# Performance work log

Measured on AMD Instinct MI355X. Metric: run time of the kernel, lower is better.

The kernel has to match this reference:

```python
import jax, jax.numpy as jnp
import numpy as np

EPS = 1e-5
GROUPS = 32


def group_norm(x, gamma, beta):
    # x: [B, C, H, W], normalize per group over (C/G, H, W)
    B, C, H, W = x.shape
    xg = x.reshape(B, GROUPS, C // GROUPS, H, W)
    mean = xg.mean(axis=(2, 3, 4), keepdims=True)
    var = xg.var(axis=(2, 3, 4), keepdims=True)
    xg = (xg - mean) * jax.lax.rsqrt(var + EPS)
    x = xg.reshape(B, C, H, W)
    return x * gamma[None, :, None, None] + beta[None, :, None, None]


def setup_inputs() -> dict:
    key = jax.random.key(0)
    ks = jax.random.split(key, 6)
    B, C, H, W = 8, 512, 64, 64
    x = jax.random.normal(ks[0], (B, C, H, W), dtype=jnp.float32)
    gamma = jnp.ones((C,), dtype=jnp.float32)
    beta = jnp.zeros((C,), dtype=jnp.float32)
    # conv1x1 weights stored as [out, in] (kernel size 1 squeezed)
    w_qkv = jax.random.normal(ks[1], (3 * C, C), dtype=jnp.float32) / np.sqrt(C)
    b_qkv = jnp.zeros((3 * C,), dtype=jnp.float32)
    w_out = jax.random.normal(ks[2], (C, C), dtype=jnp.float32) / np.sqrt(C)
    b_out = jnp.zeros((C,), dtype=jnp.float32)
    return {"x": x, "gamma": gamma, "beta": beta,
            "w_qkv": w_qkv, "b_qkv": b_qkv, "w_out": w_out, "b_out": b_out}


def reference(x, gamma, beta, w_qkv, b_qkv, w_out, b_out):
    B, C, H, W = x.shape
    N = H * W
    h = group_norm(x, gamma, beta).reshape(B, C, N)
    # conv1d kernel-size-1: channel mixing
    qkv = jnp.einsum('oc,bcn->bon', w_qkv, h) + b_qkv[None, :, None]
    q, k, v = jnp.split(qkv, 3, axis=1)  # each [B, C, N]
    scale = 1.0 / jnp.sqrt(jnp.float32(C))
    attn = jnp.einsum('bci,bcj->bij', q, k) * scale  # [B, N, N]
    attn = jax.nn.softmax(attn, axis=-1)
    out = jnp.einsum('bcj,bij->bci', v, attn)  # [B, C, N]
    out = jnp.einsum('oc,bcn->bon', w_out, out) + b_out[None, :, None]
    return x + out.reshape(B, C, H, W)
```

## Files before the change

### kernel.cpp

```cpp
#include <hip/hip_runtime.h>

#define BB 8
#define CC 512
#define NN 4096
#define GG 32
#define OQKV 1536
#define EPSV 1e-5f
#define SCALE 0.044194173824159216f

#define BATCH_STRIDE 6291456u
#define V_OFF 0u
#define Q_OFF 2097152u
#define K_OFF 4194304u

typedef unsigned short u16;
typedef unsigned int u32;
typedef __attribute__((ext_vector_type(8))) short bf16x8;
typedef __attribute__((ext_vector_type(4))) float f32x4;

__device__ __forceinline__ u16 f2bf(float f) {
  u32 u = __float_as_uint(f);
  u32 r = (u + 0x7FFFu + ((u >> 16) & 1u)) >> 16;
  return (u16)r;
}

__device__ __forceinline__ void gload_lds16(const u16* g, u16* l) {
  __builtin_amdgcn_global_load_lds(
      (const __attribute__((address_space(1))) u32*)(g),
      (__attribute__((address_space(3))) u32*)(l), 16, 0, 0);
}

__global__ __launch_bounds__(256) void gn_stats_kernel(const float* __restrict__ x,
                                                       float* __restrict__ stats) {
  const int bg = blockIdx.x;
  const float4* xp = (const float4*)(x + (size_t)bg * 16 * NN);
  const int n4 = 16 * NN / 4;
  float s = 0.f, ss = 0.f;
  for (int i = threadIdx.x; i < n4; i += 256) {
    float4 v = xp[i];
    s += v.x + v.y + v.z + v.w;
    ss += v.x * v.x + v.y * v.y + v.z * v.z + v.w * v.w;
  }
  for (int off = 32; off > 0; off >>= 1) {
    s += __shfl_down(s, off, 64);
    ss += __shfl_down(ss, off, 64);
  }
  __shared__ float rs[4], rss[4];
  const int wid = threadIdx.x >> 6, lane = threadIdx.x & 63;
  if (lane == 0) { rs[wid] = s; rss[wid] = ss; }
  __syncthreads();
  if (threadIdx.x == 0) {
    float S = rs[0] + rs[1] + rs[2] + rs[3];
    float SS = rss[0] + rss[1] + rss[2] + rss[3];
    const float invn = 1.0f / (16.0f * NN);
    float mean = S * invn;
    float var = SS * invn - mean * mean;
    stats[bg * 2] = mean;
    stats[bg * 2 + 1] = rsqrtf(var + EPSV);
  }
}

__global__ __launch_bounds__(256) void gn_transpose_kernel(
    const float* __restrict__ x, const float* __restrict__ gamma,
    const float* __restrict__ beta, const float* __restrict__ stats,
    u16* __restrict__ hT) {
  __shared__ __align__(16) u16 Ts[64 * 64];
  const int b = blockIdx.z;
  const int c0 = blockIdx.y * 64;
  const int n0 = blockIdx.x * 64;
  const int t = threadIdx.x;
  const float* xb = x + ((size_t)b * CC + c0) * NN;
#pragma unroll
  for (int it = 0; it < 2; ++it) {
    const int U = it * 256 + t;
    const int r = U >> 3, cu = U & 7;
    const int c = c0 + r;
    const int g = c >> 4;
    const float mean = stats[(b * GG + g) * 2];
    const float rstd = stats[(b * GG + g) * 2 + 1];
    const float aa = rstd * gamma[c];
    const float dd = beta[c] - mean * aa;
    const float* src = xb + (size_t)r * NN + n0 + cu * 8;
    float4 v0 = *(const float4*)src;
    float4 v1 = *(const float4*)(src + 4);
    uint4 pk;
    pk.x = (u32)f2bf(fmaf(aa, v0.x, dd)) | ((u32)f2bf(fmaf(aa, v0.y, dd)) << 16);
    pk.y = (u32)f2bf(fmaf(aa, v0.z, dd)) | ((u32)f2bf(fmaf(aa, v0.w, dd)) << 16);
    pk.z = (u32)f2bf(fmaf(aa, v1.x, dd)) | ((u32)f2bf(fmaf(aa, v1.y, dd)) << 16);
    pk.w = (u32)f2bf(fmaf(aa, v1.z, dd)) | ((u32)f2bf(fmaf(aa, v1.w, dd)) << 16);
    const int pu = cu ^ ((r >> 3) & 7);
    *(uint4*)((char*)Ts + r * 128 + pu * 16) = pk;
  }
  __syncthreads();
#pragma unroll
  for (int it = 0; it < 2; ++it) {
    const int U = it * 256 + t;
    const int n = U >> 3, cu2 = U & 7;
    bf16x8 v;
#pragma unroll
    for (int jj = 0; jj < 8; ++jj) {
      const int c = cu2 * 8 + jj;
      v[jj] = (short)Ts[c * 64 + (((n >> 3) ^ cu2) << 3) + (n & 7)];
    }
    *(bf16x8*)(hT + ((size_t)b * NN + n0 + n) * CC + c0 + cu2 * 8) = v;
  }
}

__global__ __launch_bounds__(256) void convert_w_kernel(const float* __restrict__ w,
                                                        u16* __restrict__ wb, int n8) {
  const int i = blockIdx.x * 256 + threadIdx.x;
  if (i >= n8) return;
  const float4 a = *(const float4*)(w + (size_t)i * 8);
  const float4 b = *(const float4*)(w + (size_t)i * 8 + 4);
  uint4 pk;
  pk.x = (u32)f2bf(a.x) | ((u32)f2bf(a.y) << 16);
  pk.y = (u32)f2bf(a.z) | ((u32)f2bf(a.w) << 16);
  pk.z = (u32)f2bf(b.x) | ((u32)f2bf(b.y) << 16);
  pk.w = (u32)f2bf(b.z) | ((u32)f2bf(b.w) << 16);
  *(uint4*)(wb + (size_t)i * 8) = pk;
}

__global__ __launch_bounds__(256) void qkv_mfma_kernel(
    const u16* __restrict__ hT, const u16* __restrict__ wbf,
    const float* __restrict__ bqkv, u16* __restrict__ qkv) {
  __shared__ __align__(16) u16 Asb[128 * 32 * 2];
  u16* const Bsb = Asb + 128 * 32;
  const int b = blockIdx.z;
  const int o0 = blockIdx.y * 128;
  const int n0 = blockIdx.x * 128;
  const int t = threadIdx.x;
  const int w = t >> 6;
  const int lane = t & 63;
  const int quad = lane >> 4;
  const int m16 = lane & 15;
  const int wm = w >> 1, wn = w & 1;

  const int sr = lane >> 2;
  const int gu = (lane & 3) ^ ((lane >> 3) & 3);
  const u16* gA0 = wbf + (size_t)(o0 + w * 32 + sr) * CC + gu * 8;
  const u16* gA1 = gA0 + (size_t)16 * CC;
  const u16* hTb = hT + (size_t)b * NN * CC;
  const u16* gB0 = hTb + (size_t)(n0 + w * 32 + sr) * CC + gu * 8;
  const u16* gB1 = gB0 + (size_t)16 * CC;
  u16* const lA0 = Asb + (w * 32) * 32;
  u16* const lA1 = Asb + (w * 32 + 16) * 32;
  u16* const lB0 = Bsb + (w * 32) * 32;
  u16* const lB1 = Bsb + (w * 32 + 16) * 32;

  const int sfr = (m16 >> 1) & 3;
  const u16* aP[4];
  const u16* bP[4];
#pragma unroll
  for (int mt = 0; mt < 4; ++mt)
    aP[mt] = Asb + (wm * 64 + mt * 16 + m16) * 32 + (quad ^ sfr) * 8;
#pragma unroll
  for (int ct = 0; ct < 4; ++ct)
    bP[ct] = Bsb + (wn * 64 + ct * 16 + m16) * 32 + (quad ^ sfr) * 8;

  f32x4 acc[4][4];
#pragma unroll
  for (int mt = 0; mt < 4; ++mt)
#pragma unroll
    for (int ct = 0; ct < 4; ++ct) acc[mt][ct] = (f32x4){0.f, 0.f, 0.f, 0.f};

  for (int kk = 0; kk < 16; ++kk) {
    __syncthreads();
    gload_lds16(gA0, lA0);
    gload_lds16(gA1, lA1);
    gload_lds16(gB0, lB0);
    gload_lds16(gB1, lB1);
    gA0 += 32; gA1 += 32; gB0 += 32; gB1 += 32;
    __syncthreads();
    bf16x8 af[4], bfr[4];
#pragma unroll
    for (int mt = 0; mt < 4; ++mt) af[mt] = *(const bf16x8*)aP[mt];
#pragma unroll
    for (int ct = 0; ct < 4; ++ct) bfr[ct] = *(const bf16x8*)bP[ct];
#pragma unroll
    for (int mt = 0; mt < 4; ++mt)
#pragma unroll
      for (int ct = 0; ct < 4; ++ct)
        acc[mt][ct] = __builtin_amdgcn_mfma_f32_16x16x32_bf16(af[mt], bfr[ct],
                                                              acc[mt][ct], 0, 0, 0);
  }
  __syncthreads();

  u16* qb = qkv + (size_t)b * BATCH_STRIDE;
  size_t roff;
  int lo0;
  if (o0 < 512) { roff = Q_OFF; lo0 = o0; }
  else if (o0 < 1024) { roff = K_OFF; lo0 = o0 - 512; }
  else { roff = V_OFF; lo0 = o0 - 1024; }

  u16* const scr = Asb + w * 1024;
#pragma unroll
  for (int mt = 0; mt < 4; ++mt) {
#pragma unroll
    for (int ct = 0; ct < 4; ++ct) {
#pragma unroll
      for (int i = 0; i < 4; ++i) {
        const int row = quad * 4 + i;
        const int nn = ct * 16 + m16;
        const int pu = (nn >> 3) ^ ((row & 7) ^ (row >> 3));
        scr[row * 64 + pu * 8 + (nn & 7)] =
            f2bf(acc[mt][ct][i] + bqkv[o0 + wm * 64 + mt * 16 + row]);
      }
    }
    __syncthreads();
#pragma unroll
    for (int half = 0; half < 2; ++half) {
      const int idx = half * 64 + lane;
      const int row = idx >> 3;
      const int cu = idx & 7;
      const int pu = cu ^ ((row & 7) ^ (row >> 3));
      bf16x8 vv = *(const bf16x8*)(scr + row * 64 + pu * 8);
      *(bf16x8*)(qb + roff + (size_t)(lo0 + wm * 64 + mt * 16 + row) * NN +
                 n0 + wn * 64 + cu * 8) = vv;
    }
    __syncthreads();
  }
}

__global__ __launch_bounds__(256) void transpose_qk_kernel(
    const u16* __restrict__ qkvbuf, u16* __restrict__ qT, u16* __restrict__ kT) {
  __shared__ __align__(16) u16 Ts[64 * 64];
  const int b = blockIdx.z >> 1;
  const int which = blockIdx.z & 1;
  const int c0 = blockIdx.y * 64;
  const int n0 = blockIdx.x * 64;
  const int t = threadIdx.x;
  const u16* src = qkvbuf + (size_t)b * BATCH_STRIDE + (which ? K_OFF : Q_OFF);
  u16* dst = (which ? kT : qT) + (size_t)b * (CC * NN);
#pragma unroll
  for (int it = 0; it < 2; ++it) {
    const int U = it * 256 + t;
    const int r = U >> 3, cu = U & 7;
    const int pu = cu ^ ((r >> 3) & 7);
    *(uint4*)((char*)Ts + r * 128 + pu * 16) =
        *(const uint4*)(src + (size_t)(c0 + r) * NN + n0 + cu * 8);
  }
  __syncthreads();
#pragma unroll
  for (int it = 0; it < 2; ++it) {
    const int U = it * 256 + t;
    const int n = U >> 3, cu2 = U & 7;
    bf16x8 v;
#pragma unroll
    for (int jj = 0; jj < 8; ++jj) {
      const int c = cu2 * 8 + jj;
      v[jj] = (short)Ts[c * 64 + (((n >> 3) ^ cu2) << 3) + (n & 7)];
    }
    *(bf16x8*)(dst + (size_t)(n0 + n) * CC + c0 + cu2 * 8) = v;
  }
}

__global__ __launch_bounds__(512, 2) void attn_mfma_kernel(
    u16* __restrict__ qkvbuf, const u16* __restrict__ qT, const u16* __restrict__ kT) {
  __shared__ __align__(16) u16 Kt[32 * 512];
  __shared__ __align__(16) float ps[64][36];
  __shared__ __align__(16) u16 Pb[64][40];
  __shared__ float alpha_s[64], invl_s[64];

  const int b = blockIdx.y;
  const int i0 = blockIdx.x * 64;
  const int t = threadIdx.x;
  const int w = t >> 6;
  const int lane = t & 63;
  const int quad = lane >> 4;
  const int m16 = lane & 15;
  const int mt_s = w & 3;
  const int nt_s = w >> 2;

  const u16* vb = qkvbuf + (size_t)b * BATCH_STRIDE + V_OFF;
  float* obuf = (float*)(qkvbuf + (size_t)b * BATCH_STRIDE + Q_OFF);
  const u16* qTb = qT + (size_t)b * (CC * NN);
  const u16* kTb = kT + (size_t)b * (CC * NN);

  bf16x8 qf[16];
  {
    const u16* qrow = qTb + (size_t)(i0 + mt_s * 16 + m16) * CC + quad * 8;
#pragma unroll
    for (int kc = 0; kc < 16; ++kc) qf[kc] = *(const bf16x8*)(qrow + kc * 32);
  }

  float m_r = -1e30f, l_r = 0.f;

  f32x4 oacc[4][4];
#pragma unroll
  for (int a = 0; a < 4; ++a)
#pragma unroll
    for (int c = 0; c < 4; ++c) oacc[a][c] = (f32x4){0.f, 0.f, 0.f, 0.f};

  uint4 kreg[4];
#pragma unroll
  for (int it = 0; it < 4; ++it) {
    const int j = it * 8 + w;
    const int u = lane ^ (j & 7);
    kreg[it] = *(const uint4*)(kTb + (size_t)j * CC + u * 8);
  }

  for (int j0 = 0; j0 < NN; j0 += 32) {
    __syncthreads();
#pragma unroll
    for (int it = 0; it < 4; ++it) {
      const int j = it * 8 + w;
      *(uint4*)((char*)Kt + j * 1024 + lane * 16) = kreg[it];
    }
    if (j0 + 32 < NN) {
#pragma unroll
      for (int it = 0; it < 4; ++it) {
        const int j = it * 8 + w;
        const int u = lane ^ (j & 7);
        kreg[it] = *(const uint4*)(kTb + (size_t)(j0 + 32 + j) * CC + u * 8);
      }
    }
    bf16x8 vf[4];
#pragma unroll
    for (int ct = 0; ct < 4; ++ct) {
      const int c = w * 64 + ct * 16 + m16;
      vf[ct] = *(const bf16x8*)(vb + (size_t)c * NN + j0 + quad * 8);
    }
    __syncthreads();
    f32x4 sacc = (f32x4){0.f, 0.f, 0.f, 0.f};
    {
      const int j = nt_s * 16 + m16;
      const char* krow = (const char*)Kt + j * 1024;
      const int swz = j & 7;
#pragma unroll
      for (int kc = 0; kc < 16; ++kc) {
        const int u = (kc * 4 + quad) ^ swz;
        bf16x8 kf = *(const bf16x8*)(krow + u * 16);
        sacc = __builtin_amdgcn_mfma_f32_16x16x32_bf16(qf[kc], kf, sacc, 0, 0, 0);
      }
    }
    {
      const int row = mt_s * 16 + quad * 4;
      const int col = nt_s * 16 + m16;
#pragma unroll
      for (int r = 0; r < 4; ++r) ps[row + r][col] = sacc[r] * SCALE;
    }
    __syncthreads();
    if (t < 256) {
      const int row = t >> 2, part = t & 3;
      float4 s0 = *(const float4*)&ps[row][part * 8];
      float4 s1 = *(const float4*)&ps[row][part * 8 + 4];
      float mx = fmaxf(fmaxf(fmaxf(s0.x, s0.y), fmaxf(s0.z, s0.w)),
                       fmaxf(fmaxf(s1.x, s1.y), fmaxf(s1.z, s1.w)));
      mx = fmaxf(mx, __shfl_xor(mx, 1, 64));
      mx = fmaxf(mx, __shfl_xor(mx, 2, 64));
      const float mnew = fmaxf(m_r, mx);
      const float alpha = __expf(m_r - mnew);
      float p0 = __expf(s0.x - mnew), p1 = __expf(s0.y - mnew);
      float p2 = __expf(s0.z - mnew), p3 = __expf(s0.w - mnew);
      float p4 = __expf(s1.x - mnew), p5 = __expf(s1.y - mnew);
      float p6 = __expf(s1.z - mnew), p7 = __expf(s1.w - mnew);
      float sum = ((p0 + p1) + (p2 + p3)) + ((p4 + p5) + (p6 + p7));
      sum += __shfl_xor(sum, 1, 64);
      sum += __shfl_xor(sum, 2, 64);
      l_r = l_r * alpha + sum;
      m_r = mnew;
      if (part == 0) alpha_s[row] = alpha;
      uint4 pk;
      pk.x = (u32)f2bf(p0) | ((u32)f2bf(p1) << 16);
      pk.y = (u32)f2bf(p2) | ((u32)f2bf(p3) << 16);
      pk.z = (u32)f2bf(p4) | ((u32)f2bf(p5) << 16);
      pk.w = (u32)f2bf(p6) | ((u32)f2bf(p7) << 16);
      *(uint4*)&Pb[row][part * 8] = pk;
    }
    __syncthreads();
    float4 alph[4];
#pragma unroll
    for (int mt = 0; mt < 4; ++mt)
      alph[mt] = *(const float4*)&alpha_s[mt * 16 + quad * 4];
#pragma unroll
    for (int mt = 0; mt < 4; ++mt) {
      bf16x8 pf = *(const bf16x8*)&Pb[mt * 16 + m16][quad * 8];
#pragma unroll
      for (int ct = 0; ct < 4; ++ct) {
        f32x4 o = oacc[mt][ct];
        o[0] *= alph[mt].x;
        o[1] *= alph[mt].y;
        o[2] *= alph[mt].z;
        o[3] *= alph[mt].w;
        oacc[mt][ct] = __builtin_amdgcn_mfma_f32_16x16x32_bf16(pf, vf[ct], o, 0, 0, 0);
      }
    }
  }
  if (t < 256 && (t & 3) == 0) invl_s[t >> 2] = 1.0f / l_r;
  __syncthreads();
#pragma unroll
  for (int mt = 0; mt < 4; ++mt) {
    float4 il = *(const float4*)&invl_s[mt * 16 + quad * 4];
#pragma unroll
    for (int ct = 0; ct < 4; ++ct) {
      const int c = w * 64 + ct * 16 + m16;
      float4 ov;
      ov.x = oacc[mt][ct][0] * il.x;
      ov.y = oacc[mt][ct][1] * il.y;
      ov.z = oacc[mt][ct][2] * il.z;
      ov.w = oacc[mt][ct][3] * il.w;
      *(float4*)(obuf + (size_t)c * NN + i0 + mt * 16 + quad * 4) = ov;
    }
  }
}

__global__ __launch_bounds__(256) void proj_kernel(
    const u16* __restrict__ qkvbuf, const float* __restrict__ wout,
    const float* __restrict__ bout, const float* __restrict__ x,
    float* __restrict__ out) {
  __shared__ __align__(16) float Wt[16][68];
  __shared__ __align__(16) float Ht[16][68];
  const int b = blockIdx.z;
  const int o0 = blockIdx.y * 64;
  const int n0 = blockIdx.x * 64;
  const int t = threadIdx.x;
  const int to = (t >> 4) * 4;
  const int tn = (t & 15) * 4;
  const int wo = t >> 2;
  const int wk = (t & 3) * 4;
  const int xc = t >> 4;
  const int xn = (t & 15) * 4;
  const float* ob = (const float*)(qkvbuf + (size_t)b * BATCH_STRIDE + Q_OFF);
  float acc[4][4] = {{0.f}};
  for (int kk = 0; kk < CC; kk += 16) {
    float4 wv = *(const float4*)(wout + (size_t)(o0 + wo) * CC + kk + wk);
    float4 hv = *(const float4*)(ob + (size_t)(kk + xc) * NN + n0 + xn);
    __syncthreads();
    Wt[wk + 0][wo] = wv.x;
    Wt[wk + 1][wo] = wv.y;
    Wt[wk + 2][wo] = wv.z;
    Wt[wk + 3][wo] = wv.w;
    *(float4*)&Ht[xc][xn] = hv;
    __syncthreads();
#pragma unroll
    for (int k = 0; k < 16; ++k) {
      float4 w4 = *(const float4*)&Wt[k][to];
      float4 h4 = *(const float4*)&Ht[k][tn];
      acc[0][0] = fmaf(w4.x, h4.x, acc[0][0]);
      acc[0][1] = fmaf(w4.x, h4.y, acc[0][1]);
      acc[0][2] = fmaf(w4.x, h4.z, acc[0][2]);
      acc[0][3] = fmaf(w4.x, h4.w, acc[0][3]);
      acc[1][0] = fmaf(w4.y, h4.x, acc[1][0]);
      acc[1][1] = fmaf(w4.y, h4.y, acc[1][1]);
      acc[1][2] = fmaf(w4.y, h4.z, acc[1][2]);
      acc[1][3] = fmaf(w4.y, h4.w, acc[1][3]);
      acc[2][0] = fmaf(w4.z, h4.x, acc[2][0]);
      acc[2][1] = fmaf(w4.z, h4.y, acc[2][1]);
      acc[2][2] = fmaf(w4.z, h4.z, acc[2][2]);
      acc[2][3] = fmaf(w4.z, h4.w, acc[2][3]);
      acc[3][0] = fmaf(w4.w, h4.x, acc[3][0]);
      acc[3][1] = fmaf(w4.w, h4.y, acc[3][1]);
      acc[3][2] = fmaf(w4.w, h4.z, acc[3][2]);
      acc[3][3] = fmaf(w4.w, h4.w, acc[3][3]);
    }
  }
#pragma unroll
  for (int i = 0; i < 4; ++i) {
    const int o = o0 + to + i;
    const float bias = bout[o];
    const size_t idx = ((size_t)b * CC + o) * NN + n0 + tn;
    float4 xv = *(const float4*)(x + idx);
    float4 r;
    r.x = acc[i][0] + bias + xv.x;
    r.y = acc[i][1] + bias + xv.y;
    r.z = acc[i][2] + bias + xv.z;
    r.w = acc[i][3] + bias + xv.w;
    *(float4*)(out + idx) = r;
  }
}

extern "C" void kernel_launch(void* const* d_in, const int* in_sizes, int n_in,
                              void* d_out, int out_size, void* d_ws, size_t ws_size,
                              hipStream_t stream) {
  const float* x = (const float*)d_in[0];
  const float* gamma = (const float*)d_in[1];
  const float* beta = (const float*)d_in[2];
  const float* wqkv = (const float*)d_in[3];
  const float* bqkv = (const float*)d_in[4];
  const float* wout = (const float*)d_in[5];
  const float* bout = (const float*)d_in[6];
  float* out = (float*)d_out;

  char* ws = (char*)d_ws;
  float* stats = (float*)ws;
  u16* qkv = (u16*)(ws + 4096);
  u16* qT = (u16*)(ws + 4096 + (size_t)BB * OQKV * NN * 2);
  u16* kT = qT + (size_t)BB * CC * NN;
  u16* hT = qT;
  u16* wbf = kT;

  gn_stats_kernel<<<BB * GG, 256, 0, stream>>>(x, stats);
  gn_transpose_kernel<<<dim3(NN / 64, CC / 64, BB), 256, 0, stream>>>(
      x, gamma, beta, stats, hT);
  convert_w_kernel<<<(OQKV * CC / 8 + 255) / 256, 256, 0, stream>>>(
      wqkv, wbf, OQKV * CC / 8);
  qkv_mfma_kernel<<<dim3(NN / 128, OQKV / 128, BB), 256, 0, stream>>>(
      hT, wbf, bqkv, qkv);
  transpose_qk_kernel<<<dim3(NN / 64, CC / 64, BB * 2), 256, 0, stream>>>(qkv, qT, kT);
  attn_mfma_kernel<<<dim3(NN / 64, BB), 512, 0, stream>>>(qkv, qT, kT);
  proj_kernel<<<dim3(NN / 64, CC / 64, BB), 256, 0, stream>>>(qkv, wout, bout, x, out);
}
```

Before: 1.531 ms.

## Restructure attention: per-wave 16-query rows, double-buffered K/V LDS via direct loads

The attention kernel now has each wave own 16 query rows across all 512 channels, which doubles the query tile to 128 per block and halves the grid. K and V tiles are double-buffered in LDS using global_load_lds, and the softmax runs in registers with cross-lane shuffles instead of through a shared score buffer. Rescaling of the accumulator is skipped when no row's max changed. This removes most block-level barriers and the LDS round trip for scores, and reuses each K/V tile across twice as many queries. In exchange it holds 32 accumulator tiles per thread, which raises register pressure and may cut occupancy.

Result: slower. 2.332 ms (+52.3%).

```diff
diff --git a/kernel.cpp b/kernel.cpp
--- a/kernel.cpp
+++ b/kernel.cpp
@@ -22,6 +22,10 @@
   u32 u = __float_as_uint(f);
   u32 r = (u + 0x7FFFu + ((u >> 16) & 1u)) >> 16;
   return (u16)r;
+}
+
+__device__ __forceinline__ u32 pack2bf(float a, float b) {
+  return (u32)f2bf(a) | ((u32)f2bf(b) << 16);
 }
 
 __device__ __forceinline__ void gload_lds16(const u16* g, u16* l) {
@@ -84,10 +88,10 @@
     float4 v0 = *(const float4*)src;
     float4 v1 = *(const float4*)(src + 4);
     uint4 pk;
-    pk.x = (u32)f2bf(fmaf(aa, v0.x, dd)) | ((u32)f2bf(fmaf(aa, v0.y, dd)) << 16);
-    pk.y = (u32)f2bf(fmaf(aa, v0.z, dd)) | ((u32)f2bf(fmaf(aa, v0.w, dd)) << 16);
-    pk.z = (u32)f2bf(fmaf(aa, v1.x, dd)) | ((u32)f2bf(fmaf(aa, v1.y, dd)) << 16);
-    pk.w = (u32)f2bf(fmaf(aa, v1.z, dd)) | ((u32)f2bf(fmaf(aa, v1.w, dd)) << 16);
+    pk.x = pack2bf(fmaf(aa, v0.x, dd), fmaf(aa, v0.y, dd));
+    pk.y = pack2bf(fmaf(aa, v0.z, dd), fmaf(aa, v0.w, dd));
+    pk.z = pack2bf(fmaf(aa, v1.x, dd), fmaf(aa, v1.y, dd));
+    pk.w = pack2bf(fmaf(aa, v1.z, dd), fmaf(aa, v1.w, dd));
     const int pu = cu ^ ((r >> 3) & 7);
     *(uint4*)((char*)Ts + r * 128 + pu * 16) = pk;
   }
@@ -113,10 +117,10 @@
   const float4 a = *(const float4*)(w + (size_t)i * 8);
   const float4 b = *(const float4*)(w + (size_t)i * 8 + 4);
   uint4 pk;
-  pk.x = (u32)f2bf(a.x) | ((u32)f2bf(a.y) << 16);
-  pk.y = (u32)f2bf(a.z) | ((u32)f2bf(a.w) << 16);
-  pk.z = (u32)f2bf(b.x) | ((u32)f2bf(b.y) << 16);
-  pk.w = (u32)f2bf(b.z) | ((u32)f2bf(b.w) << 16);
+  pk.x = pack2bf(a.x, a.y);
+  pk.y = pack2bf(a.z, a.w);
+  pk.z = pack2bf(b.x, b.y);
+  pk.w = pack2bf(b.z, b.w);
   *(uint4*)(wb + (size_t)i * 8) = pk;
 }
 
@@ -256,151 +260,156 @@
 
 __global__ __launch_bounds__(512, 2) void attn_mfma_kernel(
     u16* __restrict__ qkvbuf, const u16* __restrict__ qT, const u16* __restrict__ kT) {
-  __shared__ __align__(16) u16 Kt[32 * 512];
-  __shared__ __align__(16) float ps[64][36];
-  __shared__ __align__(16) u16 Pb[64][40];
-  __shared__ float alpha_s[64], invl_s[64];
+  __shared__ __align__(16) u16 smem[70656];
+  u16* const KtA = smem;
+  u16* const KtB = smem + 16384;
+  u16* const VtA = smem + 32768;
+  u16* const VtB = smem + 49152;
+  u16* const Pbase = smem + 65536;
 
   const int b = blockIdx.y;
-  const int i0 = blockIdx.x * 64;
+  const int i0 = blockIdx.x * 128;
   const int t = threadIdx.x;
   const int w = t >> 6;
   const int lane = t & 63;
   const int quad = lane >> 4;
   const int m16 = lane & 15;
-  const int mt_s = w & 3;
-  const int nt_s = w >> 2;
 
   const u16* vb = qkvbuf + (size_t)b * BATCH_STRIDE + V_OFF;
   float* obuf = (float*)(qkvbuf + (size_t)b * BATCH_STRIDE + Q_OFF);
   const u16* qTb = qT + (size_t)b * (CC * NN);
   const u16* kTb = kT + (size_t)b * (CC * NN);
+  u16* const myP = Pbase + w * 640;
+
+  const int kswz = (lane ^ 0) * 0;  (void)kswz;
+  const int vsrcu = ((lane & 3) ^ ((lane >> 2) & 3)) * 8;
+  const int vrow = lane >> 2;
+
+#pragma unroll
+  for (int it = 0; it < 4; ++it) {
+    const int j = it * 8 + w;
+    gload_lds16(kTb + (size_t)j * CC + (lane ^ (j & 7)) * 8, KtA + j * 512 + lane * 8);
+  }
+#pragma unroll
+  for (int it = 0; it < 4; ++it) {
+    const int seg = it * 8 + w;
+    const int c = seg * 16 + vrow;
+    gload_lds16(vb + (size_t)c * NN + vsrcu, VtA + seg * 512 + lane * 8);
+  }
 
   bf16x8 qf[16];
   {
-    const u16* qrow = qTb + (size_t)(i0 + mt_s * 16 + m16) * CC + quad * 8;
+    const u16* qrow = qTb + (size_t)(i0 + w * 16 + m16) * CC + quad * 8;
 #pragma unroll
     for (int kc = 0; kc < 16; ++kc) qf[kc] = *(const bf16x8*)(qrow + kc * 32);
   }
 
   float m_r = -1e30f, l_r = 0.f;
-
-  f32x4 oacc[4][4];
-#pragma unroll
-  for (int a = 0; a < 4; ++a)
-#pragma unroll
-    for (int c = 0; c < 4; ++c) oacc[a][c] = (f32x4){0.f, 0.f, 0.f, 0.f};
-
-  uint4 kreg[4];
-#pragma unroll
-  for (int it = 0; it < 4; ++it) {
-    const int j = it * 8 + w;
-    const int u = lane ^ (j & 7);
-    kreg[it] = *(const uint4*)(kTb + (size_t)j * CC + u * 8);
-  }
-
-  for (int j0 = 0; j0 < NN; j0 += 32) {
-    __syncthreads();
-#pragma unroll
-    for (int it = 0; it < 4; ++it) {
-      const int j = it * 8 + w;
-      *(uint4*)((char*)Kt + j * 1024 + lane * 16) = kreg[it];
-    }
-    if (j0 + 32 < NN) {
+  f32x4 oacc[32];
+#pragma unroll
+  for (int ct = 0; ct < 32; ++ct) oacc[ct] = (f32x4){0.f, 0.f, 0.f, 0.f};
+
+  __syncthreads();
+
+  for (int jt = 0; jt < NN / 32; ++jt) {
+    const int cur = jt & 1;
+    const u16* Ktc = cur ? KtB : KtA;
+    const u16* Vtc = cur ? VtB : VtA;
+    if (jt + 1 < NN / 32) {
+      u16* Ktn = cur ? KtA : KtB;
+      u16* Vtn = cur ? VtA : VtB;
+      const int j0n = (jt + 1) * 32;
 #pragma unroll
       for (int it = 0; it < 4; ++it) {
         const int j = it * 8 + w;
-        const int u = lane ^ (j & 7);
-        kreg[it] = *(const uint4*)(kTb + (size_t)(j0 + 32 + j) * CC + u * 8);
+        gload_lds16(kTb + (size_t)(j0n + j) * CC + (lane ^ (j & 7)) * 8,
+                    Ktn + j * 512 + lane * 8);
       }
-    }
-    bf16x8 vf[4];
-#pragma unroll
-    for (int ct = 0; ct < 4; ++ct) {
-      const int c = w * 64 + ct * 16 + m16;
-      vf[ct] = *(const bf16x8*)(vb + (size_t)c * NN + j0 + quad * 8);
-    }
-    __syncthreads();
-    f32x4 sacc = (f32x4){0.f, 0.f, 0.f, 0.f};
+#pragma unroll
+      for (int it = 0; it < 4; ++it) {
+        const int seg = it * 8 + w;
+        const int c = seg * 16 + vrow;
+        gload_lds16(vb + (size_t)c * NN + j0n + vsrcu, Vtn + seg * 512 + lane * 8);
+      }
+    }
+    f32x4 s0 = (f32x4){0.f, 0.f, 0.f, 0.f};
+    f32x4 s1 = (f32x4){0.f, 0.f, 0.f, 0.f};
     {
-      const int j = nt_s * 16 + m16;
-      const char* krow = (const char*)Kt + j * 1024;
-      const int swz = j & 7;
+      const u16* k0 = Ktc + m16 * 512;
+      const u16* k1 = Ktc + (16 + m16) * 512;
+      const int sz = m16 & 7;
 #pragma unroll
       for (int kc = 0; kc < 16; ++kc) {
-        const int u = (kc * 4 + quad) ^ swz;
-        bf16x8 kf = *(const bf16x8*)(krow + u * 16);
-        sacc = __builtin_amdgcn_mfma_f32_16x16x32_bf16(qf[kc], kf, sacc, 0, 0, 0);
+        const int u = (((kc * 4 + quad) ^ sz)) * 8;
+        bf16x8 ka = *(const bf16x8*)(k0 + u);
+        bf16x8 kb = *(const bf16x8*)(k1 + u);
+        s0 = __builtin_amdgcn_mfma_f32_16x16x32_bf16(ka, qf[kc], s0, 0, 0, 0);
+        s1 = __builtin_amdgcn_mfma_f32_16x16x32_bf16(kb, qf[kc], s1, 0, 0, 0);
       }
     }
-    {
-      const int row = mt_s * 16 + quad * 4;
-      const int col = nt_s * 16 + m16;
-#pragma unroll
-      for (int r = 0; r < 4; ++r) ps[row + r][col] = sacc[r] * SCALE;
-    }
-    __syncthreads();
-    if (t < 256) {
-      const int row = t >> 2, part = t & 3;
-      float4 s0 = *(const float4*)&ps[row][part * 8];
-      float4 s1 = *(const float4*)&ps[row][part * 8 + 4];
-      float mx = fmaxf(fmaxf(fmaxf(s0.x, s0.y), fmaxf(s0.z, s0.w)),
-                       fmaxf(fmaxf(s1.x, s1.y), fmaxf(s1.z, s1.w)));
-      mx = fmaxf(mx, __shfl_xor(mx, 1, 64));
-      mx = fmaxf(mx, __shfl_xor(mx, 2, 64));
-      const float mnew = fmaxf(m_r, mx);
-      const float alpha = __expf(m_r - mnew);
-      float p0 = __expf(s0.x - mnew), p1 = __expf(s0.y - mnew);
-      float p2 = __expf(s0.z - mnew), p3 = __expf(s0.w - mnew);
-      float p4 = __expf(s1.x - mnew), p5 = __expf(s1.y - mnew);
-      float p6 = __expf(s1.z - mnew), p7 = __expf(s1.w - mnew);
-      float sum = ((p0 + p1) + (p2 + p3)) + ((p4 + p5) + (p6 + p7));
-      sum += __shfl_xor(sum, 1, 64);
-      sum += __shfl_xor(sum, 2, 64);
-      l_r = l_r * alpha + sum;
-      m_r = mnew;
-      if (part == 0) alpha_s[row] = alpha;
-      uint4 pk;
-      pk.x = (u32)f2bf(p0) | ((u32)f2bf(p1) << 16);
-      pk.y = (u32)f2bf(p2) | ((u32)f2bf(p3) << 16);
-      pk.z = (u32)f2bf(p4) | ((u32)f2bf(p5) << 16);
-      pk.w = (u32)f2bf(p6) | ((u32)f2bf(p7) << 16);
-      *(uint4*)&Pb[row][part * 8] = pk;
-    }
-    __syncthreads();
-    float4 alph[4];
-#pragma unroll
-    for (int mt = 0; mt < 4; ++mt)
-      alph[mt] = *(const float4*)&alpha_s[mt * 16 + quad * 4];
-#pragma unroll
-    for (int mt = 0; mt < 4; ++mt) {
-      bf16x8 pf = *(const bf16x8*)&Pb[mt * 16 + m16][quad * 8];
-#pragma unroll
-      for (int ct = 0; ct < 4; ++ct) {
-        f32x4 o = oacc[mt][ct];
-        o[0] *= alph[mt].x;
-        o[1] *= alph[mt].y;
-        o[2] *= alph[mt].z;
-        o[3] *= alph[mt].w;
-        oacc[mt][ct] = __builtin_amdgcn_mfma_f32_16x16x32_bf16(pf, vf[ct], o, 0, 0, 0);
+    float p0 = s0[0] * SCALE, p1 = s0[1] * SCALE, p2 = s0[2] * SCALE, p3 = s0[3] * SCALE;
+    float p4 = s1[0] * SCALE, p5 = s1[1] * SCALE, p6 = s1[2] * SCALE, p7 = s1[3] * SCALE;
+    float mx = fmaxf(fmaxf(fmaxf(p0, p1), fmaxf(p2, p3)),
+                     fmaxf(fmaxf(p4, p5), fmaxf(p6, p7)));
+    mx = fmaxf(mx, __shfl_xor(mx, 16));
+    mx = fmaxf(mx, __shfl_xor(mx, 32));
+    const float mold = m_r;
+    const float mnew = fmaxf(mold, mx);
+    m_r = mnew;
+    const float alpha = __expf(mold - mnew);
+    p0 = __expf(p0 - mnew); p1 = __expf(p1 - mnew);
+    p2 = __expf(p2 - mnew); p3 = __expf(p3 - mnew);
+    p4 = __expf(p4 - mnew); p5 = __expf(p5 - mnew);
+    p6 = __expf(p6 - mnew); p7 = __expf(p7 - mnew);
+    float sum = ((p0 + p1) + (p2 + p3)) + ((p4 + p5) + (p6 + p7));
+    sum += __shfl_xor(sum, 16);
+    sum += __shfl_xor(sum, 32);
+    l_r = l_r * alpha + sum;
+    uint2 pw0, pw1;
+    pw0.x = pack2bf(p0, p1); pw0.y = pack2bf(p2, p3);
+    pw1.x = pack2bf(p4, p5); pw1.y = pack2bf(p6, p7);
+    *(uint2*)(myP + m16 * 40 + quad * 4) = pw0;
+    *(uint2*)(myP + m16 * 40 + 16 + quad * 4) = pw1;
+    asm volatile("s_waitcnt lgkmcnt(0)" ::: "memory");
+    bf16x8 pf = *(const bf16x8*)(myP + m16 * 40 + quad * 8);
+    const float a0 = __shfl(alpha, quad * 4 + 0);
+    const float a1 = __shfl(alpha, quad * 4 + 1);
+    const float a2 = __shfl(alpha, quad * 4 + 2);
+    const float a3 = __shfl(alpha, quad * 4 + 3);
+    const u16* vbase = Vtc + m16 * 32 + (quad ^ (m16 & 3)) * 8;
+    const bool nores = __all(mnew == mold);
+    if (nores) {
+#pragma unroll
+      for (int ct = 0; ct < 32; ++ct) {
+        bf16x8 vf = *(const bf16x8*)(vbase + ct * 512);
+        oacc[ct] = __builtin_amdgcn_mfma_f32_16x16x32_bf16(pf, vf, oacc[ct], 0, 0, 0);
       }
-    }
-  }
-  if (t < 256 && (t & 3) == 0) invl_s[t >> 2] = 1.0f / l_r;
-  __syncthreads();
-#pragma unroll
-  for (int mt = 0; mt < 4; ++mt) {
-    float4 il = *(const float4*)&invl_s[mt * 16 + quad * 4];
-#pragma unroll
-    for (int ct = 0; ct < 4; ++ct) {
-      const int c = w * 64 + ct * 16 + m16;
-      float4 ov;
-      ov.x = oacc[mt][ct][0] * il.x;
-      ov.y = oacc[mt][ct][1] * il.y;
-      ov.z = oacc[mt][ct][2] * il.z;
-      ov.w = oacc[mt][ct][3] * il.w;
-      *(float4*)(obuf + (size_t)c * NN + i0 + mt * 16 + quad * 4) = ov;
-    }
+    } else {
+#pragma unroll
+      for (int ct = 0; ct < 32; ++ct) {
+        bf16x8 vf = *(const bf16x8*)(vbase + ct * 512);
+        f32x4 o = oacc[ct];
+        o[0] *= a0; o[1] *= a1; o[2] *= a2; o[3] *= a3;
+        oacc[ct] = __builtin_amdgcn_mfma_f32_16x16x32_bf16(pf, vf, o, 0, 0, 0);
+      }
+    }
+    __syncthreads();
+  }
+  const float invl = 1.0f / l_r;
+  const float il0 = __shfl(invl, quad * 4 + 0);
+  const float il1 = __shfl(invl, quad * 4 + 1);
+  const float il2 = __shfl(invl, quad * 4 + 2);
+  const float il3 = __shfl(invl, quad * 4 + 3);
+  const size_t ncol = i0 + w * 16 + quad * 4;
+#pragma unroll
+  for (int ct = 0; ct < 32; ++ct) {
+    const int c = ct * 16 + m16;
+    float4 ov;
+    ov.x = oacc[ct][0] * il0;
+    ov.y = oacc[ct][1] * il1;
+    ov.z = oacc[ct][2] * il2;
+    ov.w = oacc[ct][3] * il3;
+    *(float4*)(obuf + (size_t)c * NN + ncol) = ov;
   }
 }
 
@@ -497,6 +506,6 @@
   qkv_mfma_kernel<<<dim3(NN / 128, OQKV / 128, BB), 256, 0, stream>>>(
       hT, wbf, bqkv, qkv);
   transpose_qk_kernel<<<dim3(NN / 64, CC / 64, BB * 2), 256, 0, stream>>>(qkv, qT, kT);
-  attn_mfma_kernel<<<dim3(NN / 64, BB), 512, 0, stream>>>(qkv, qT, kT);
+  attn_mfma_kernel<<<dim3(NN / 128, BB), 512, 0, stream>>>(qkv, qT, kT);
   proj_kernel<<<dim3(NN / 64, CC / 64, BB), 256, 0, stream>>>(qkv, wout, bout, x, out);
 }
```
